# Optimization experiments

Measured on AMD Instinct MI355X. Metric: run time of the kernel, lower is better.

The kernel has to match this reference:

```python
import jax, jax.numpy as jnp
import numpy as np
from itertools import product

DIM = 384
HEADS = 8
DIM_HEAD = 64
INNER = HEADS * DIM_HEAD  # 512
KS = 3                    # kernel_size (attention window)
PAD = KS // 2
W_WIN = KS * KS           # 9
SCALE = DIM_HEAD ** -0.5


def setup_inputs() -> dict:
    key = jax.random.key(0)
    k1, k2, k3, k4, k5 = jax.random.split(key, 5)
    B, H, W = 4, 56, 56
    x = jax.random.normal(k1, (B, DIM, H, W), dtype=jnp.float32)
    # 1x1 conv weights stored as (out_ch, in_ch)
    Wq = jax.random.normal(k2, (INNER, DIM), dtype=jnp.float32) * (DIM ** -0.5)
    Wkv = jax.random.normal(k3, (2 * INNER, DIM), dtype=jnp.float32) * (DIM ** -0.5)
    Wo = jax.random.normal(k4, (DIM, INNER), dtype=jnp.float32) * (INNER ** -0.5)
    bo = jax.random.normal(k5, (DIM,), dtype=jnp.float32) * 0.01
    return {"x": x, "Wq": Wq, "Wkv": Wkv, "Wo": Wo, "bo": bo}


def _conv1x1(x, w):
    # x: (B,Cin,H,W), w: (Cout,Cin) -> (B,Cout,H,W)
    return jnp.einsum('bchw,oc->bohw', x, w)


def reference(x, Wq, Wkv, Wo, bo):
    B, C, H, W = x.shape
    q = _conv1x1(x, Wq)                       # (B, INNER, H, W)
    kv = _conv1x1(x, Wkv)                     # (B, 2*INNER, H, W)
    k, v = jnp.split(kv, 2, axis=1)
    # split channels heads-major, matching torch reshape (B, heads, dh, H, W)
    q = q.reshape(B, HEADS, DIM_HEAD, H, W)
    k = k.reshape(B, HEADS, DIM_HEAD, H, W)
    v = v.reshape(B, HEADS, DIM_HEAD, H, W)
    # zero-pad spatial dims (matches F.unfold zero padding: padded taps get logit 0)
    k_pad = jnp.pad(k, ((0, 0), (0, 0), (0, 0), (PAD, PAD), (PAD, PAD)))
    v_pad = jnp.pad(v, ((0, 0), (0, 0), (0, 0), (PAD, PAD), (PAD, PAD)))
    offsets = list(product(range(KS), range(KS)))  # row-major = unfold order
    # dots: (B, heads, H, W, w)
    dots = jnp.stack([
        jnp.einsum('bhdxy,bhdxy->bhxy', q, k_pad[:, :, :, i:i + H, j:j + W])
        for (i, j) in offsets
    ], axis=-1) * SCALE
    attn = jax.nn.softmax(dots, axis=-1)      # softmax over the 9-tap window
    # weighted sum of shifted v: (B, heads, dh, H, W)
    out = sum(
        attn[:, :, None, :, :, w_idx] * v_pad[:, :, :, i:i + H, j:j + W]
        for w_idx, (i, j) in enumerate(offsets)
    )
    out = out.reshape(B, INNER, H, W)
    return _conv1x1(out, Wo) + bo[None, :, None, None]
```

## Files before the change

kernel.cpp:

```cpp
#include <hip/hip_runtime.h>


#define HW 3136
#define WIMG 56
#define QKV_CH 1536
#define SCALE 0.125f
#define SLEN 200

typedef __bf16 bf16x8_t __attribute__((ext_vector_type(8)));
typedef float f32x4_t __attribute__((ext_vector_type(4)));

__device__ __forceinline__ float bf2f(unsigned short u) {
    return __uint_as_float(((unsigned int)u) << 16);
}
__device__ __forceinline__ unsigned short f2bf(float f) {
    unsigned int u = __float_as_uint(f);
    u += 0x7FFFu + ((u >> 16) & 1u);
    return (unsigned short)(u >> 16);
}
__device__ __forceinline__ int gpos(int g, int row) { return (g + ((row >> 1) & 3)) & 3; }

__global__ __launch_bounds__(256) void cvt_w(
    const float* __restrict__ Wq, const float* __restrict__ Wkv,
    const float* __restrict__ Wo,
    unsigned short* __restrict__ wT, unsigned short* __restrict__ wob)
{
    const int i = blockIdx.x * 256 + threadIdx.x;
    if (i < 73728) {
        const int g = i & 3;
        const int idx3 = i >> 2;
        const int o128 = idx3 & 127;
        const int rest = idx3 >> 7;
        const int kb = rest % 12, oblk = rest / 12;
        const int o = oblk * 128 + o128;
        const int k0 = kb * 32 + g * 8;
        const float* src = (o < 512) ? (Wq + (size_t)o * 384 + k0)
                                     : (Wkv + (size_t)(o - 512) * 384 + k0);
        const float4 v0 = *reinterpret_cast<const float4*>(src);
        const float4 v1 = *reinterpret_cast<const float4*>(src + 4);
        uint4 u;
        u.x = (unsigned int)f2bf(v0.x) | ((unsigned int)f2bf(v0.y) << 16);
        u.y = (unsigned int)f2bf(v0.z) | ((unsigned int)f2bf(v0.w) << 16);
        u.z = (unsigned int)f2bf(v1.x) | ((unsigned int)f2bf(v1.y) << 16);
        u.w = (unsigned int)f2bf(v1.z) | ((unsigned int)f2bf(v1.w) << 16);
        reinterpret_cast<uint4*>(wT)[i] = u;
    } else {
        const int j = i - 73728;
        const float4 v0 = reinterpret_cast<const float4*>(Wo)[j * 2];
        const float4 v1 = reinterpret_cast<const float4*>(Wo)[j * 2 + 1];
        uint4 u;
        u.x = (unsigned int)f2bf(v0.x) | ((unsigned int)f2bf(v0.y) << 16);
        u.y = (unsigned int)f2bf(v0.z) | ((unsigned int)f2bf(v0.w) << 16);
        u.z = (unsigned int)f2bf(v1.x) | ((unsigned int)f2bf(v1.y) << 16);
        u.w = (unsigned int)f2bf(v1.z) | ((unsigned int)f2bf(v1.w) << 16);
        reinterpret_cast<uint4*>(wob)[j] = u;
    }
}

__global__ __launch_bounds__(256) void cvtT_x(
    const float* __restrict__ x, unsigned short* __restrict__ xT)
{
    __shared__ unsigned short Tl[64 * 36];
    const int sblk = blockIdx.x, kblk = blockIdx.y, b = blockIdx.z;
    const int t = threadIdx.x;

    if (sblk == 49) {
        unsigned short* dst = xT + (((size_t)b * 25 + 24) * 12 + kblk) * 4096 + 2048;
        *reinterpret_cast<uint4*>(dst + t * 8) = (uint4){0, 0, 0, 0};
        return;
    }

    const float* xp = x + ((size_t)b * 384 + (size_t)kblk * 32) * HW + sblk * 64;
    const int c = t >> 3;
#pragma unroll
    for (int i = 0; i < 2; i++) {
        const int sc = (t & 7) + 8 * i;
        const float4 v = *reinterpret_cast<const float4*>(xp + (size_t)c * HW + sc * 4);
        const int s4 = sc * 4;
        Tl[(s4 + 0) * 36 + c] = f2bf(v.x);
        Tl[(s4 + 1) * 36 + c] = f2bf(v.y);
        Tl[(s4 + 2) * 36 + c] = f2bf(v.z);
        Tl[(s4 + 3) * 36 + c] = f2bf(v.w);
    }
    __syncthreads();

    const int row = t >> 2, gran = t & 3;
    const uint2 lo = *reinterpret_cast<const uint2*>(&Tl[row * 36 + gran * 8]);
    const uint2 hi = *reinterpret_cast<const uint2*>(&Tl[row * 36 + gran * 8 + 4]);
    uint4 o; o.x = lo.x; o.y = lo.y; o.z = hi.x; o.w = hi.y;
    unsigned short* dst = xT + (((size_t)b * 25 + (sblk >> 1)) * 12 + kblk) * 4096
                        + (sblk & 1) * 2048;
    *reinterpret_cast<uint4*>(dst + t * 8) = o;
}

__global__ __launch_bounds__(256) void gemm1(
    const unsigned short* __restrict__ xT,
    const unsigned short* __restrict__ wT,
    unsigned short* __restrict__ qkv)
{
    __shared__ __align__(16) unsigned short A_lds[128 * 32];
    __shared__ __align__(16) unsigned short B_lds[128 * 32];

    const int sblk = blockIdx.x;
    const int oblk = blockIdx.y;
    const int b  = blockIdx.z;
    const int t  = threadIdx.x;
    const int lane = t & 63, w = t >> 6;
    const int quad = lane >> 4, mrow = lane & 15;
    const int wm = w >> 1, wn = w & 1;

    const unsigned short* wsrc = wT + ((size_t)oblk * 12) * 4096;
    const unsigned short* xsrc = xT + (((size_t)b * 25 + sblk) * 12) * 4096;

    f32x4_t acc[4][4];
#pragma unroll
    for (int m = 0; m < 4; m++)
#pragma unroll
        for (int n = 0; n < 4; n++) acc[m][n] = (f32x4_t){0.f, 0.f, 0.f, 0.f};

    for (int kb = 0; kb < 12; kb++) {
        const uint4 a0 = *reinterpret_cast<const uint4*>(wsrc + (size_t)kb * 4096 + t * 8);
        const uint4 a1 = *reinterpret_cast<const uint4*>(wsrc + (size_t)kb * 4096 + 2048 + t * 8);
        const uint4 b0 = *reinterpret_cast<const uint4*>(xsrc + (size_t)kb * 4096 + t * 8);
        const uint4 b1 = *reinterpret_cast<const uint4*>(xsrc + (size_t)kb * 4096 + 2048 + t * 8);

        __syncthreads();
        *reinterpret_cast<uint4*>(A_lds + t * 8) = a0;
        *reinterpret_cast<uint4*>(A_lds + 2048 + t * 8) = a1;
        *reinterpret_cast<uint4*>(B_lds + t * 8) = b0;
        *reinterpret_cast<uint4*>(B_lds + 2048 + t * 8) = b1;
        __syncthreads();

        bf16x8_t af[4], bf[4];
#pragma unroll
        for (int m = 0; m < 4; m++)
            af[m] = *reinterpret_cast<const bf16x8_t*>(&A_lds[(wm * 64 + m * 16 + mrow) * 32 + quad * 8]);
#pragma unroll
        for (int n = 0; n < 4; n++)
            bf[n] = *reinterpret_cast<const bf16x8_t*>(&B_lds[(wn * 64 + n * 16 + mrow) * 32 + quad * 8]);
#pragma unroll
        for (int m = 0; m < 4; m++)
#pragma unroll
            for (int n = 0; n < 4; n++)
                acc[m][n] = __builtin_amdgcn_mfma_f32_16x16x32_bf16(af[m], bf[n], acc[m][n], 0, 0, 0);
    }

    const int o0 = oblk * 128 + wm * 64;
    const int s0 = sblk * 128 + wn * 64;
    unsigned short* outb = qkv + (size_t)b * QKV_CH * HW;
#pragma unroll
    for (int m = 0; m < 4; m++)
#pragma unroll
        for (int n = 0; n < 4; n++) {
            const int ss = s0 + n * 16 + mrow;
            if (ss < HW) {
#pragma unroll
                for (int r = 0; r < 4; r++) {
                    const int oo = o0 + m * 16 + quad * 4 + r;
                    outb[(size_t)oo * HW + ss] = f2bf(acc[m][n][r]);
                }
            }
        }
}

__global__ __launch_bounds__(256) void gemm3(
    const unsigned short* __restrict__ ao,
    const unsigned short* __restrict__ Wb,
    const float* __restrict__ bias,
    float* __restrict__ out)
{
    __shared__ __align__(16) unsigned short A_lds[128 * 32];
    __shared__ __align__(16) unsigned short B_lds[64 * 32];

    const int s0 = blockIdx.x * 64;
    const int o0 = blockIdx.y * 128;
    const int b  = blockIdx.z;
    const int t  = threadIdx.x;
    const int lane = t & 63, w = t >> 6;
    const int quad = lane >> 4, mrow = lane & 15;

    const int ar = t >> 2, ag = t & 3;
    const int bs = t & 63, bg = t >> 6;

    const unsigned short* xp = ao + (size_t)b * 512 * HW + s0 + bs;
    const unsigned short* wr0 = Wb + (size_t)(o0 + ar) * 512;
    const unsigned short* wr1 = Wb + (size_t)(o0 + 64 + ar) * 512;

    f32x4_t acc[2][4];
#pragma unroll
    for (int m = 0; m < 2; m++)
#pragma unroll
        for (int nt = 0; nt < 4; nt++) acc[m][nt] = (f32x4_t){0.f, 0.f, 0.f, 0.f};

    for (int k0 = 0; k0 < 512; k0 += 32) {
        const uint4 a0 = *reinterpret_cast<const uint4*>(wr0 + k0 + ag * 8);
        const uint4 a1 = *reinterpret_cast<const uint4*>(wr1 + k0 + ag * 8);
        __align__(16) unsigned short bv[8];
#pragma unroll
        for (int j = 0; j < 8; j++)
            bv[j] = xp[(size_t)(k0 + bg * 8 + j) * HW];

        __syncthreads();
        *reinterpret_cast<uint4*>(&A_lds[ar * 32 + gpos(ag, ar) * 8]) = a0;
        *reinterpret_cast<uint4*>(&A_lds[(64 + ar) * 32 + gpos(ag, 64 + ar) * 8]) = a1;
        *reinterpret_cast<uint4*>(&B_lds[bs * 32 + gpos(bg, bs) * 8]) =
            *reinterpret_cast<const uint4*>(bv);
        __syncthreads();

        bf16x8_t bfr[4];
#pragma unroll
        for (int nt = 0; nt < 4; nt++) {
            const int srow = nt * 16 + mrow;
            bfr[nt] = *reinterpret_cast<const bf16x8_t*>(&B_lds[srow * 32 + gpos(quad, srow) * 8]);
        }
#pragma unroll
        for (int m = 0; m < 2; m++) {
            const int orow = w * 32 + m * 16 + mrow;
            const bf16x8_t af = *reinterpret_cast<const bf16x8_t*>(&A_lds[orow * 32 + gpos(quad, orow) * 8]);
#pragma unroll
            for (int nt = 0; nt < 4; nt++)
                acc[m][nt] = __builtin_amdgcn_mfma_f32_16x16x32_bf16(af, bfr[nt], acc[m][nt], 0, 0, 0);
        }
    }

#pragma unroll
    for (int m = 0; m < 2; m++)
#pragma unroll
        for (int nt = 0; nt < 4; nt++)
#pragma unroll
            for (int r = 0; r < 4; r++) {
                const int oo = o0 + w * 32 + m * 16 + quad * 4 + r;
                const int ss = s0 + nt * 16 + mrow;
                out[(size_t)b * 384 * HW + (size_t)oo * HW + ss] = acc[m][nt][r] + bias[oo];
            }
}

__global__ __launch_bounds__(256) void natt2(
    const unsigned short* __restrict__ qkv,
    unsigned short* __restrict__ ao)
{
    __shared__ __align__(16) unsigned short smem[2 * 64 * SLEN];
    unsigned short* Kl = smem;
    unsigned short* Vl = smem + 64 * SLEN;
    float* dred = reinterpret_cast<float*>(smem);

    const int t = threadIdx.x, lane = t & 63, w = t >> 6;
    const int s0 = blockIdx.x * 64;
    const int s  = s0 + lane;
    const int h  = blockIdx.y, b = blockIdx.z;
    const int y  = s / WIMG, xx = s % WIMG;

    const size_t hbase = (size_t)b * QKV_CH * HW + (size_t)(h * 64) * HW;
    const unsigned short* kg = qkv + hbase + (size_t)512 * HW;
    const unsigned short* vg = qkv + hbase + (size_t)1024 * HW;

#pragma unroll
    for (int i = 0; i < 6; i++) {
        const int f = i * 256 + t;
        const int d = f / 24, j = f % 24;
        int g = s0 - 64 + j * 8;
        g = min(max(g, 0), HW - 8);
        const uint4 k4 = *reinterpret_cast<const uint4*>(kg + (size_t)d * HW + g);
        const uint4 v4 = *reinterpret_cast<const uint4*>(vg + (size_t)d * HW + g);
        *reinterpret_cast<uint4*>(&Kl[d * SLEN + j * 8]) = k4;
        *reinterpret_cast<uint4*>(&Vl[d * SLEN + j * 8]) = v4;
    }

    int   off9[9];
    float msk[9];
#pragma unroll
    for (int ty = 0; ty < 3; ty++)
#pragma unroll
        for (int tx = 0; tx < 3; tx++) {
            const int tap = ty * 3 + tx;
            const int ny = y + ty - 1, nx = xx + tx - 1;
            const bool v = (ny >= 0) && (ny < WIMG) && (nx >= 0) && (nx < WIMG);
            off9[tap] = v ? ((ty - 1) * WIMG + (tx - 1)) : 0;
            msk[tap]  = v ? 1.f : 0.f;
        }

    __syncthreads();

    const unsigned short* qp = qkv + hbase + s;
    float dots[9];
#pragma unroll
    for (int tp = 0; tp < 9; tp++) dots[tp] = 0.f;
#pragma unroll 4
    for (int dd = 0; dd < 16; dd++) {
        const int d = w * 16 + dd;
        const float qv = bf2f(qp[(size_t)d * HW]);
        const int bi = d * SLEN + lane + 64;
#pragma unroll
        for (int tp = 0; tp < 9; tp++)
            dots[tp] += qv * bf2f(Kl[bi + off9[tp]]);
    }

    __syncthreads();
#pragma unroll
    for (int tp = 0; tp < 9; tp++) dred[(tp * 4 + w) * 64 + lane] = dots[tp];
    __syncthreads();

    float mx = -1e30f, dt[9];
#pragma unroll
    for (int tp = 0; tp < 9; tp++) {
        const float sum = dred[(tp * 4 + 0) * 64 + lane] + dred[(tp * 4 + 1) * 64 + lane] +
                          dred[(tp * 4 + 2) * 64 + lane] + dred[(tp * 4 + 3) * 64 + lane];
        dt[tp] = msk[tp] * (sum * SCALE);
        mx = fmaxf(mx, dt[tp]);
    }
    float se = 0.f, w9[9];
#pragma unroll
    for (int tp = 0; tp < 9; tp++) { w9[tp] = __expf(dt[tp] - mx); se += w9[tp]; }
    const float inv = 1.f / se;
#pragma unroll
    for (int tp = 0; tp < 9; tp++) w9[tp] *= inv * msk[tp];

    unsigned short* aop = ao + (size_t)b * 512 * HW + (size_t)(h * 64) * HW + s;
#pragma unroll 4
    for (int dd = 0; dd < 16; dd++) {
        const int d = w * 16 + dd;
        const int bi = d * SLEN + lane + 64;
        float o = 0.f;
#pragma unroll
        for (int tp = 0; tp < 9; tp++)
            o += w9[tp] * bf2f(Vl[bi + off9[tp]]);
        aop[(size_t)d * HW] = f2bf(o);
    }
}

extern "C" void kernel_launch(void* const* d_in, const int* in_sizes, int n_in,
                              void* d_out, int out_size, void* d_ws, size_t ws_size,
                              hipStream_t stream) {
    const float* x   = (const float*)d_in[0];
    const float* Wq  = (const float*)d_in[1];
    const float* Wkv = (const float*)d_in[2];
    const float* Wo  = (const float*)d_in[3];
    const float* bo  = (const float*)d_in[4];
    float* out = (float*)d_out;

    unsigned short* xT   = (unsigned short*)d_ws;
    unsigned short* wT   = xT + (size_t)4915200;
    unsigned short* wob  = wT + (size_t)589824;
    unsigned short* qkvb = wob + (size_t)196608;
    unsigned short* aob  = qkvb + (size_t)4 * QKV_CH * HW;

    cvt_w<<<dim3(384), 256, 0, stream>>>(Wq, Wkv, Wo, wT, wob);
    cvtT_x<<<dim3(50, 12, 4), 256, 0, stream>>>(x, xT);

    gemm1<<<dim3(25, 12, 4), 256, 0, stream>>>(xT, wT, qkvb);
    natt2<<<dim3(49, 8, 4), 256, 0, stream>>>(qkvb, aob);
    gemm3<<<dim3(49, 3, 4), 256, 0, stream>>>(aob, wob, bo, out);
}
```

Measured before the change: 149.5 us.

## Write attention output in tiled GEMM-ready layout and simplify output projection loads

The attention kernel now packs its per-thread outputs into 16-element vectors and writes them into a blocked layout (spatial block × k-block × row × 32). The output projection GEMM can then read A and B tiles with contiguous 16-byte loads instead of strided scalar gathers. The Wo weights are pre-blocked the same way in the conversion kernel, and the swizzle is dropped. The GEMM warp tiling changes to 64x32 per warp. This targets the uncoalesced gathers and strided 2-byte stores in the final projection, at the risk of LDS bank conflicts now that the swizzle is gone.

```diff
diff --git a/kernel.cpp b/kernel.cpp
--- a/kernel.cpp
+++ b/kernel.cpp
@@ -18,12 +18,11 @@
     u += 0x7FFFu + ((u >> 16) & 1u);
     return (unsigned short)(u >> 16);
 }
-__device__ __forceinline__ int gpos(int g, int row) { return (g + ((row >> 1) & 3)) & 3; }
 
 __global__ __launch_bounds__(256) void cvt_w(
     const float* __restrict__ Wq, const float* __restrict__ Wkv,
     const float* __restrict__ Wo,
-    unsigned short* __restrict__ wT, unsigned short* __restrict__ wob)
+    unsigned short* __restrict__ wT, unsigned short* __restrict__ wT3)
 {
     const int i = blockIdx.x * 256 + threadIdx.x;
     if (i < 73728) {
@@ -46,14 +45,21 @@
         reinterpret_cast<uint4*>(wT)[i] = u;
     } else {
         const int j = i - 73728;
-        const float4 v0 = reinterpret_cast<const float4*>(Wo)[j * 2];
-        const float4 v1 = reinterpret_cast<const float4*>(Wo)[j * 2 + 1];
+        const int g = j & 3;
+        const int idx3 = j >> 2;
+        const int o128 = idx3 & 127;
+        const int rest = idx3 >> 7;
+        const int kb = rest % 16, oblk = rest / 16;
+        const int o = oblk * 128 + o128;
+        const float* src = Wo + (size_t)o * 512 + kb * 32 + g * 8;
+        const float4 v0 = *reinterpret_cast<const float4*>(src);
+        const float4 v1 = *reinterpret_cast<const float4*>(src + 4);
         uint4 u;
         u.x = (unsigned int)f2bf(v0.x) | ((unsigned int)f2bf(v0.y) << 16);
         u.y = (unsigned int)f2bf(v0.z) | ((unsigned int)f2bf(v0.w) << 16);
         u.z = (unsigned int)f2bf(v1.x) | ((unsigned int)f2bf(v1.y) << 16);
         u.w = (unsigned int)f2bf(v1.z) | ((unsigned int)f2bf(v1.w) << 16);
-        reinterpret_cast<uint4*>(wob)[j] = u;
+        reinterpret_cast<uint4*>(wT3)[j] = u;
     }
 }
 
@@ -163,81 +169,9 @@
         }
 }
 
-__global__ __launch_bounds__(256) void gemm3(
-    const unsigned short* __restrict__ ao,
-    const unsigned short* __restrict__ Wb,
-    const float* __restrict__ bias,
-    float* __restrict__ out)
-{
-    __shared__ __align__(16) unsigned short A_lds[128 * 32];
-    __shared__ __align__(16) unsigned short B_lds[64 * 32];
-
-    const int s0 = blockIdx.x * 64;
-    const int o0 = blockIdx.y * 128;
-    const int b  = blockIdx.z;
-    const int t  = threadIdx.x;
-    const int lane = t & 63, w = t >> 6;
-    const int quad = lane >> 4, mrow = lane & 15;
-
-    const int ar = t >> 2, ag = t & 3;
-    const int bs = t & 63, bg = t >> 6;
-
-    const unsigned short* xp = ao + (size_t)b * 512 * HW + s0 + bs;
-    const unsigned short* wr0 = Wb + (size_t)(o0 + ar) * 512;
-    const unsigned short* wr1 = Wb + (size_t)(o0 + 64 + ar) * 512;
-
-    f32x4_t acc[2][4];
-#pragma unroll
-    for (int m = 0; m < 2; m++)
-#pragma unroll
-        for (int nt = 0; nt < 4; nt++) acc[m][nt] = (f32x4_t){0.f, 0.f, 0.f, 0.f};
-
-    for (int k0 = 0; k0 < 512; k0 += 32) {
-        const uint4 a0 = *reinterpret_cast<const uint4*>(wr0 + k0 + ag * 8);
-        const uint4 a1 = *reinterpret_cast<const uint4*>(wr1 + k0 + ag * 8);
-        __align__(16) unsigned short bv[8];
-#pragma unroll
-        for (int j = 0; j < 8; j++)
-            bv[j] = xp[(size_t)(k0 + bg * 8 + j) * HW];
-
-        __syncthreads();
-        *reinterpret_cast<uint4*>(&A_lds[ar * 32 + gpos(ag, ar) * 8]) = a0;
-        *reinterpret_cast<uint4*>(&A_lds[(64 + ar) * 32 + gpos(ag, 64 + ar) * 8]) = a1;
-        *reinterpret_cast<uint4*>(&B_lds[bs * 32 + gpos(bg, bs) * 8]) =
-            *reinterpret_cast<const uint4*>(bv);
-        __syncthreads();
-
-        bf16x8_t bfr[4];
-#pragma unroll
-        for (int nt = 0; nt < 4; nt++) {
-            const int srow = nt * 16 + mrow;
-            bfr[nt] = *reinterpret_cast<const bf16x8_t*>(&B_lds[srow * 32 + gpos(quad, srow) * 8]);
-        }
-#pragma unroll
-        for (int m = 0; m < 2; m++) {
-            const int orow = w * 32 + m * 16 + mrow;
-            const bf16x8_t af = *reinterpret_cast<const bf16x8_t*>(&A_lds[orow * 32 + gpos(quad, orow) * 8]);
-#pragma unroll
-            for (int nt = 0; nt < 4; nt++)
-                acc[m][nt] = __builtin_amdgcn_mfma_f32_16x16x32_bf16(af, bfr[nt], acc[m][nt], 0, 0, 0);
-        }
-    }
-
-#pragma unroll
-    for (int m = 0; m < 2; m++)
-#pragma unroll
-        for (int nt = 0; nt < 4; nt++)
-#pragma unroll
-            for (int r = 0; r < 4; r++) {
-                const int oo = o0 + w * 32 + m * 16 + quad * 4 + r;
-                const int ss = s0 + nt * 16 + mrow;
-                out[(size_t)b * 384 * HW + (size_t)oo * HW + ss] = acc[m][nt][r] + bias[oo];
-            }
-}
-
 __global__ __launch_bounds__(256) void natt2(
     const unsigned short* __restrict__ qkv,
-    unsigned short* __restrict__ ao)
+    unsigned short* __restrict__ aoT)
 {
     __shared__ __align__(16) unsigned short smem[2 * 64 * SLEN];
     unsigned short* Kl = smem;
@@ -245,7 +179,8 @@
     float* dred = reinterpret_cast<float*>(smem);
 
     const int t = threadIdx.x, lane = t & 63, w = t >> 6;
-    const int s0 = blockIdx.x * 64;
+    const int sblk = blockIdx.x;
+    const int s0 = sblk * 64;
     const int s  = s0 + lane;
     const int h  = blockIdx.y, b = blockIdx.z;
     const int y  = s / WIMG, xx = s % WIMG;
@@ -315,7 +250,7 @@
 #pragma unroll
     for (int tp = 0; tp < 9; tp++) w9[tp] *= inv * msk[tp];
 
-    unsigned short* aop = ao + (size_t)b * 512 * HW + (size_t)(h * 64) * HW + s;
+    __align__(16) unsigned short ov[16];
 #pragma unroll 4
     for (int dd = 0; dd < 16; dd++) {
         const int d = w * 16 + dd;
@@ -324,8 +259,79 @@
 #pragma unroll
         for (int tp = 0; tp < 9; tp++)
             o += w9[tp] * bf2f(Vl[bi + off9[tp]]);
-        aop[(size_t)d * HW] = f2bf(o);
-    }
+        ov[dd] = f2bf(o);
+    }
+    unsigned short* dst = aoT + (((size_t)(b * 49 + sblk)) * 16 + (h * 2 + (w >> 1))) * 2048
+                        + lane * 32 + (w & 1) * 16;
+    *reinterpret_cast<uint4*>(dst)     = *reinterpret_cast<const uint4*>(ov);
+    *reinterpret_cast<uint4*>(dst + 8) = *reinterpret_cast<const uint4*>(ov + 8);
+}
+
+__global__ __launch_bounds__(256) void gemm3(
+    const unsigned short* __restrict__ aoT,
+    const unsigned short* __restrict__ wT3,
+    const float* __restrict__ bias,
+    float* __restrict__ out)
+{
+    __shared__ __align__(16) unsigned short A_lds[128 * 32];
+    __shared__ __align__(16) unsigned short B_lds[64 * 32];
+
+    const int sblk = blockIdx.x;
+    const int oblk = blockIdx.y;
+    const int b  = blockIdx.z;
+    const int t  = threadIdx.x;
+    const int lane = t & 63, w = t >> 6;
+    const int quad = lane >> 4, mrow = lane & 15;
+    const int wm = w >> 1, wn = w & 1;
+
+    const unsigned short* asrc = wT3 + (size_t)oblk * 16 * 4096;
+    const unsigned short* bsrc = aoT + ((size_t)(b * 49 + sblk)) * 16 * 2048;
+
+    f32x4_t acc[4][2];
+#pragma unroll
+    for (int m = 0; m < 4; m++)
+#pragma unroll
+        for (int n = 0; n < 2; n++) acc[m][n] = (f32x4_t){0.f, 0.f, 0.f, 0.f};
+
+    for (int kb = 0; kb < 16; kb++) {
+        const uint4 a0 = *reinterpret_cast<const uint4*>(asrc + (size_t)kb * 4096 + t * 8);
+        const uint4 a1 = *reinterpret_cast<const uint4*>(asrc + (size_t)kb * 4096 + 2048 + t * 8);
+        const uint4 b0 = *reinterpret_cast<const uint4*>(bsrc + (size_t)kb * 2048 + t * 8);
+
+        __syncthreads();
+        *reinterpret_cast<uint4*>(A_lds + t * 8) = a0;
+        *reinterpret_cast<uint4*>(A_lds + 2048 + t * 8) = a1;
+        *reinterpret_cast<uint4*>(B_lds + t * 8) = b0;
+        __syncthreads();
+
+        bf16x8_t af[4], bf[2];
+#pragma unroll
+        for (int m = 0; m < 4; m++)
+            af[m] = *reinterpret_cast<const bf16x8_t*>(&A_lds[(wm * 64 + m * 16 + mrow) * 32 + quad * 8]);
+#pragma unroll
+        for (int n = 0; n < 2; n++)
+            bf[n] = *reinterpret_cast<const bf16x8_t*>(&B_lds[(wn * 32 + n * 16 + mrow) * 32 + quad * 8]);
+#pragma unroll
+        for (int m = 0; m < 4; m++)
+#pragma unroll
+            for (int n = 0; n < 2; n++)
+                acc[m][n] = __builtin_amdgcn_mfma_f32_16x16x32_bf16(af[m], bf[n], acc[m][n], 0, 0, 0);
+    }
+
+    const int o0 = oblk * 128 + wm * 64;
+    const int s0 = sblk * 64 + wn * 32;
+    float* outb = out + (size_t)b * 384 * HW;
+#pragma unroll
+    for (int m = 0; m < 4; m++)
+#pragma unroll
+        for (int n = 0; n < 2; n++) {
+            const int ss = s0 + n * 16 + mrow;
+#pragma unroll
+            for (int r = 0; r < 4; r++) {
+                const int oo = o0 + m * 16 + quad * 4 + r;
+                outb[(size_t)oo * HW + ss] = acc[m][n][r] + bias[oo];
+            }
+        }
 }
 
 extern "C" void kernel_launch(void* const* d_in, const int* in_sizes, int n_in,
@@ -340,14 +346,14 @@
 
     unsigned short* xT   = (unsigned short*)d_ws;
     unsigned short* wT   = xT + (size_t)4915200;
-    unsigned short* wob  = wT + (size_t)589824;
-    unsigned short* qkvb = wob + (size_t)196608;
-    unsigned short* aob  = qkvb + (size_t)4 * QKV_CH * HW;
-
-    cvt_w<<<dim3(384), 256, 0, stream>>>(Wq, Wkv, Wo, wT, wob);
+    unsigned short* wT3  = wT + (size_t)589824;
+    unsigned short* qkvb = wT3 + (size_t)196608;
+    unsigned short* aoT  = qkvb + (size_t)4 * QKV_CH * HW;
+
+    cvt_w<<<dim3(384), 256, 0, stream>>>(Wq, Wkv, Wo, wT, wT3);
     cvtT_x<<<dim3(50, 12, 4), 256, 0, stream>>>(x, xT);
 
     gemm1<<<dim3(25, 12, 4), 256, 0, stream>>>(xT, wT, qkvb);
-    natt2<<<dim3(49, 8, 4), 256, 0, stream>>>(qkvb, aob);
-    gemm3<<<dim3(49, 3, 4), 256, 0, stream>>>(aob, wob, bo, out);
-}
+    natt2<<<dim3(49, 8, 4), 256, 0, stream>>>(qkvb, aoT);
+    gemm3<<<dim3(49, 3, 4), 256, 0, stream>>>(aoT, wT3, bo, out);
+}
```

Result: faster. 145.5 us (-2.7%).
